# Performance work log

Measured on AMD Instinct MI355X. Metric: run time of the kernel, lower is better.

## Reference

```python
import jax, jax.numpy as jnp
import numpy as np

N_NODES = 100000
N_EDGES = 1600000
N_LABEL = 200000
HID = 128
OUT = 5


def setup_inputs() -> dict:
    key = jax.random.key(0)
    k1, k2, k3, k4, k5 = jax.random.split(key, 5)
    x = jax.random.normal(k1, (N_NODES, HID), dtype=jnp.float32)
    edge_index = jax.random.randint(k2, (2, N_EDGES), 0, N_NODES, dtype=jnp.int64)
    edge_label_index = jax.random.randint(k3, (2, N_LABEL), 0, N_NODES, dtype=jnp.int64)
    W_gcn = jax.random.normal(k4, (HID, HID), dtype=jnp.float32) / np.sqrt(HID)
    b_gcn = jnp.zeros((HID,), dtype=jnp.float32)
    W_lin = jax.random.normal(k5, (2 * HID, OUT), dtype=jnp.float32) / np.sqrt(2 * HID)
    b_lin = jnp.zeros((OUT,), dtype=jnp.float32)
    return {"x": x, "edge_index": edge_index, "edge_label_index": edge_label_index,
            "W_gcn": W_gcn, "b_gcn": b_gcn, "W_lin": W_lin, "b_lin": b_lin}


def _gcn_conv(x, edge_index, W, b):
    # PyG GCNConv defaults: add self-loops, symmetric normalization,
    # linear transform first, then scatter-add of norm * x[src] into dst.
    n = x.shape[0]
    loop = jnp.arange(n, dtype=edge_index.dtype)
    src = jnp.concatenate([edge_index[0], loop])  # [E+N]
    dst = jnp.concatenate([edge_index[1], loop])  # [E+N]
    xw = x @ W  # [N, H]
    ones = jnp.ones(src.shape[0], dtype=x.dtype)
    deg = jax.ops.segment_sum(ones, dst, num_segments=n)  # in-degree incl self-loop
    dinv = jnp.where(deg > 0, jax.lax.rsqrt(deg), 0.0)
    norm = dinv[src] * dinv[dst]  # [E+N]
    msgs = xw[src] * norm[:, None]  # [E+N, H] gather + scale
    out = jax.ops.segment_sum(msgs, dst, num_segments=n)  # scatter-add
    return out + b


def reference(x, edge_index, edge_label_index, W_gcn, b_gcn, W_lin, b_lin):
    h = _gcn_conv(x, edge_index, W_gcn, b_gcn)  # [N, H]
    drug_emb = h[edge_label_index[0]]  # [E_label, H]
    prot_emb = h[edge_label_index[1]]  # [E_label, H]
    edge_emb = jnp.concatenate([drug_emb, prot_emb], axis=1)  # [E_label, 2H]
    return edge_emb @ W_lin + b_lin  # [E_label, OUT]
```

## Files before the change

kernel.cpp:

```cpp
#include <hip/hip_runtime.h>

#define N_NODES 100000
#define N_EDGES 1600000
#define N_LABEL 200000
#define HID 128
#define OUT 5

#define NBUCK 391
#define EPB   2048
#define NBLK_E 782
#define PREC_BLKS 9


__device__ inline void bf2x(unsigned u, float& lo, float& hi) {
    lo = __uint_as_float(u << 16);
    hi = __uint_as_float(u & 0xffff0000u);
}
__device__ inline unsigned pack2(float a, float b) {
    unsigned ua = __float_as_uint(a), ub = __float_as_uint(b);
    ua = (ua + 0x7fffu + ((ua >> 16) & 1u)) >> 16;
    ub = (ub + 0x7fffu + ((ub >> 16) & 1u)) & 0xffff0000u;
    return ua | ub;
}

__global__ __launch_bounds__(256) void k_hist(const int* __restrict__ ei,
                                              int* __restrict__ hist,
                                              const float* __restrict__ Wg,
                                              const float* __restrict__ bg,
                                              const float* __restrict__ Wl,
                                              float* __restrict__ G) {
    const int t = threadIdx.x, b = blockIdx.x;
    if (b >= NBLK_E) {
        int o = (b - NBLK_E) * 256 + t;
        if (o < 129 * 16) {
            int r = o >> 4, jj = o & 15;
            float acc = 0.f;
            if (jj < 2 * OUT) {
                const int half = (jj >= OUT);
                const int j = half ? jj - OUT : jj;
                for (int c = 0; c < HID; ++c) {
                    float w2 = Wl[(half * HID + c) * OUT + j];
                    float a = (r < HID) ? Wg[r * HID + c] : bg[c];
                    acc += a * w2;
                }
            }
            G[o] = acc;
        }
        return;
    }
    __shared__ int h[NBUCK];
    for (int i = t; i < NBUCK; i += 256) h[i] = 0;
    __syncthreads();
    const int e0 = b * EPB;
#pragma unroll
    for (int i = 0; i < 8; ++i) {
        int e = e0 + i * 256 + t;
        if (e < N_EDGES) atomicAdd(&h[ei[N_EDGES + e] >> 8], 1);
    }
    __syncthreads();
    for (int i = t; i < NBUCK; i += 256) hist[i * NBLK_E + b] = h[i];
}

__global__ __launch_bounds__(256) void k_scanb(int* __restrict__ hist,
                                               int* __restrict__ btot,
                                               int* __restrict__ bbase,
                                               int* __restrict__ total) {
    __shared__ int part[256];
    const int b = blockIdx.x, t = threadIdx.x;
    int* row = hist + b * NBLK_E;
    const int lo = t * 4, hi = min(lo + 4, NBLK_E);
    int v[4]; int s = 0;
    for (int i = lo; i < hi; ++i) { v[i - lo] = row[i]; s += v[i - lo]; }
    part[t] = s;
    __syncthreads();
#pragma unroll
    for (int off = 1; off < 256; off <<= 1) {
        int a = (t >= off) ? part[t - off] : 0;
        __syncthreads();
        part[t] += a;
        __syncthreads();
    }
    int run = part[t] - s;
    for (int i = lo; i < hi; ++i) { int x = v[i - lo]; row[i] = run; run += x; }
    if (t == 255) {
        int tot = part[255];
        btot[b] = tot;
        bbase[b] = atomicAdd(total, tot);
    }
}

__global__ __launch_bounds__(256) void k_part(const int* __restrict__ ei,
                                              const int* __restrict__ hist,
                                              const int* __restrict__ bbase,
                                              unsigned* __restrict__ bedge) {
    __shared__ int cur[NBUCK];
    const int t = threadIdx.x, b = blockIdx.x;
    for (int i = t; i < NBUCK; i += 256) cur[i] = bbase[i] + hist[i * NBLK_E + b];
    __syncthreads();
    const int e0 = b * EPB;
#pragma unroll
    for (int i = 0; i < 8; ++i) {
        int e = e0 + i * 256 + t;
        if (e < N_EDGES) {
            int dst = ei[N_EDGES + e];
            unsigned src = (unsigned)ei[e];
            int pos = atomicAdd(&cur[dst >> 8], 1);
            bedge[pos] = src | ((unsigned)(dst & 255) << 20);
        }
    }
}

__global__ __launch_bounds__(256) void k_build(const unsigned* __restrict__ bedge,
                                               const int* __restrict__ bbase,
                                               const int* __restrict__ btot,
                                               int* __restrict__ csr,
                                               int2* __restrict__ seg,
                                               float* __restrict__ dinv) {
    __shared__ int cnt[256];
    __shared__ int nb[256];
    __shared__ int cursor[256];
    const int b = blockIdx.x, t = threadIdx.x;
    const int base = bbase[b];
    const int size = btot[b];
    cnt[t] = 0;
    __syncthreads();
    for (int i = t; i < size; i += 256) atomicAdd(&cnt[bedge[base + i] >> 20], 1);
    __syncthreads();
    const int c = cnt[t];
    nb[t] = c;
    __syncthreads();
#pragma unroll
    for (int off = 1; off < 256; off <<= 1) {
        int a = (t >= off) ? nb[t - off] : 0;
        __syncthreads();
        nb[t] += a;
        __syncthreads();
    }
    const int myBase = nb[t] - c;
    cursor[t] = myBase;
    __syncthreads();
    for (int i = t; i < size; i += 256) {
        unsigned v = bedge[base + i];
        int pos = atomicAdd(&cursor[v >> 20], 1);
        csr[base + pos] = (int)(v & 0xFFFFFu);
    }
    const int n = b * 256 + t;
    if (n < N_NODES) {
        seg[n] = make_int2(base + myBase, c);
        dinv[n] = rsqrtf((float)(c + 1));
    }
}

__global__ __launch_bounds__(256) void k_t(const float* __restrict__ x,
                                           const float* __restrict__ G,
                                           const float* __restrict__ dinv,
                                           unsigned* __restrict__ t16) {
    __shared__ float Gs[HID * 11];
    const int tid = threadIdx.x;
    for (int o = tid; o < HID * 10; o += 256) {
        int k = o / 10, j = o - k * 10;
        Gs[k * 11 + j] = G[k * 16 + j];
    }
    __syncthreads();

    int gid = blockIdx.x * 256 + tid;
    int n = gid >> 4;
    int i = gid & 15;

    float xv[8];
#pragma unroll
    for (int m = 0; m < 8; ++m) xv[m] = x[(size_t)n * HID + i + 16 * m];

    float p[10];
#pragma unroll
    for (int j = 0; j < 10; ++j) p[j] = 0.f;
#pragma unroll
    for (int m = 0; m < 8; ++m) {
        const float* g = &Gs[(i + 16 * m) * 11];
#pragma unroll
        for (int j = 0; j < 10; ++j) p[j] += xv[m] * g[j];
    }
#pragma unroll
    for (int off = 1; off < 16; off <<= 1) {
#pragma unroll
        for (int j = 0; j < 10; ++j) p[j] += __shfl_xor(p[j], off);
    }
    float va = (i == 0) ? p[0] : (i == 1) ? p[2] : (i == 2) ? p[4] : (i == 3) ? p[6] : p[8];
    float vb = (i == 0) ? p[1] : (i == 1) ? p[3] : (i == 2) ? p[5] : (i == 3) ? p[7] : p[9];
    float di = dinv[n];
    if (i < 5)      t16[(size_t)n * 8 + i] = pack2(di * va, di * vb);
    else if (i < 8) t16[(size_t)n * 8 + i] = 0u;
}

__global__ __launch_bounds__(256) void k_pullt(const unsigned* __restrict__ t16,
                                               const int2* __restrict__ seg,
                                               const int* __restrict__ csr,
                                               const float* __restrict__ dinv,
                                               const float* __restrict__ G,
                                               float* __restrict__ proj) {
    const int gid = blockIdx.x * 256 + threadIdx.x;
    const int n = gid >> 6;
    const int lane = gid & 63;
    const int e2 = lane >> 3;
    const int i = lane & 7;

    float aLo = 0.f, aHi = 0.f;
    if (e2 == 0) {
        bf2x(t16[(size_t)n * 8 + i], aLo, aHi);
    }

    const int2 sg = seg[n];
    const int beg = sg.x, deg = sg.y;

    for (int base = 0; base < deg; base += 64) {
        const int cnt = min(64, deg - base);
        int myIdx = (lane < cnt) ? csr[beg + base + lane] : 0;
        for (int j = 0; j * 8 < cnt; ++j) {
            int e = j * 8 + e2;
            int s = __shfl(myIdx, e);
            unsigned u = 0u;
            if (e < cnt) u = t16[(size_t)s * 8 + i];
            float lo, hi;
            bf2x(u, lo, hi);
            aLo += lo; aHi += hi;
        }
    }

    aLo += __shfl_xor(aLo, 8);  aHi += __shfl_xor(aHi, 8);
    aLo += __shfl_xor(aLo, 16); aHi += __shfl_xor(aHi, 16);
    aLo += __shfl_xor(aLo, 32); aHi += __shfl_xor(aHi, 32);

    if (lane < 5) {
        float di = dinv[n];
        float2 c0 = ((const float2*)(G + HID * 16))[lane];
        float2 r;
        r.x = di * aLo + c0.x;
        r.y = di * aHi + c0.y;
        *(float2*)&proj[(size_t)n * 16 + 2 * lane] = r;
    }
}

__global__ __launch_bounds__(256) void k_link2(const int* __restrict__ eli,
                                               const float* __restrict__ proj,
                                               const float* __restrict__ bl,
                                               float* __restrict__ out) {
    int t = blockIdx.x * 256 + threadIdx.x;
    int l = t >> 3, o = t & 7;
    if (l >= N_LABEL || o >= OUT) return;
    int d = eli[l];
    int p = eli[N_LABEL + l];
    out[l * OUT + o] = proj[d * 16 + o] + proj[p * 16 + OUT + o] + bl[o];
}

extern "C" void kernel_launch(void* const* d_in, const int* in_sizes, int n_in,
                              void* d_out, int out_size, void* d_ws, size_t ws_size,
                              hipStream_t stream) {
    const float* x     = (const float*)d_in[0];
    const int*   ei    = (const int*)d_in[1];
    const int*   eli   = (const int*)d_in[2];
    const float* W_gcn = (const float*)d_in[3];
    const float* b_gcn = (const float*)d_in[4];
    const float* W_lin = (const float*)d_in[5];
    const float* b_lin = (const float*)d_in[6];
    float* out = (float*)d_out;

    unsigned* t16    = (unsigned*)d_ws;
    float* proj      = (float*)(t16 + (size_t)N_NODES * 8);
    float* G         = proj + (size_t)N_NODES * 16;
    float* dinv      = G + 129 * 16;
    unsigned* bedge  = (unsigned*)(dinv + N_NODES);
    int*   csr       = (int*)(bedge + N_EDGES);
    int2*  seg       = (int2*)(csr + N_EDGES);
    int*   hist      = (int*)(seg + N_NODES);
    int*   btot      = hist + NBUCK * NBLK_E;
    int*   bbase     = btot + NBUCK;
    int*   total     = bbase + NBUCK;

    hipMemsetAsync(total, 0, sizeof(int), stream);

    k_hist<<<NBLK_E + PREC_BLKS, 256, 0, stream>>>(ei, hist, W_gcn, b_gcn, W_lin, G);
    k_scanb<<<NBUCK, 256, 0, stream>>>(hist, btot, bbase, total);
    k_part<<<NBLK_E, 256, 0, stream>>>(ei, hist, bbase, bedge);
    k_build<<<NBUCK, 256, 0, stream>>>(bedge, bbase, btot, csr, seg, dinv);
    k_t<<<N_NODES * 16 / 256, 256, 0, stream>>>(x, G, dinv, t16);
    k_pullt<<<N_NODES * 64 / 256, 256, 0, stream>>>(t16, seg, csr, dinv, G, proj);
    k_link2<<<(N_LABEL * 8 + 255) / 256, 256, 0, stream>>>(eli, proj, b_lin, out);
}
```

Before: 128.9 us.

## Replace CSR build and pull gather with bucketed shared-memory atomic accumulation

Drops the per-node CSR construction. Degrees are now counted from the dst-bucketed edge list, and aggregation becomes a per-bucket kernel that adds fp32 source rows into a 128-node shared-memory accumulator with LDS atomics. The bucket size shrinks from 256 to 128 nodes, which doubles the bucket count, and the bf16 packing of the projected features is replaced by full fp32 rows of 16 floats. This removes one scatter pass and the CSR/seg arrays, in exchange for doubled gather bytes per edge, shared-memory atomic contention, and only 782 aggregation blocks.

```diff
diff --git a/kernel.cpp b/kernel.cpp
--- a/kernel.cpp
+++ b/kernel.cpp
@@ -6,22 +6,13 @@
 #define HID 128
 #define OUT 5
 
-#define NBUCK 391
+#define BSH   7
+#define BSZ   128
+#define NBUCK 782
 #define EPB   2048
 #define NBLK_E 782
 #define PREC_BLKS 9
 
-
-__device__ inline void bf2x(unsigned u, float& lo, float& hi) {
-    lo = __uint_as_float(u << 16);
-    hi = __uint_as_float(u & 0xffff0000u);
-}
-__device__ inline unsigned pack2(float a, float b) {
-    unsigned ua = __float_as_uint(a), ub = __float_as_uint(b);
-    ua = (ua + 0x7fffu + ((ua >> 16) & 1u)) >> 16;
-    ub = (ub + 0x7fffu + ((ub >> 16) & 1u)) & 0xffff0000u;
-    return ua | ub;
-}
 
 __global__ __launch_bounds__(256) void k_hist(const int* __restrict__ ei,
                                               int* __restrict__ hist,
@@ -55,7 +46,7 @@
 #pragma unroll
     for (int i = 0; i < 8; ++i) {
         int e = e0 + i * 256 + t;
-        if (e < N_EDGES) atomicAdd(&h[ei[N_EDGES + e] >> 8], 1);
+        if (e < N_EDGES) atomicAdd(&h[ei[N_EDGES + e] >> BSH], 1);
     }
     __syncthreads();
     for (int i = t; i < NBUCK; i += 256) hist[i * NBLK_E + b] = h[i];
@@ -104,57 +95,33 @@
         if (e < N_EDGES) {
             int dst = ei[N_EDGES + e];
             unsigned src = (unsigned)ei[e];
-            int pos = atomicAdd(&cur[dst >> 8], 1);
-            bedge[pos] = src | ((unsigned)(dst & 255) << 20);
+            int pos = atomicAdd(&cur[dst >> BSH], 1);
+            bedge[pos] = src | ((unsigned)(dst & (BSZ - 1)) << 20);
         }
     }
 }
 
-__global__ __launch_bounds__(256) void k_build(const unsigned* __restrict__ bedge,
-                                               const int* __restrict__ bbase,
-                                               const int* __restrict__ btot,
-                                               int* __restrict__ csr,
-                                               int2* __restrict__ seg,
-                                               float* __restrict__ dinv) {
-    __shared__ int cnt[256];
-    __shared__ int nb[256];
-    __shared__ int cursor[256];
+__global__ __launch_bounds__(256) void k_deg(const unsigned* __restrict__ bedge,
+                                             const int* __restrict__ bbase,
+                                             const int* __restrict__ btot,
+                                             float* __restrict__ dinv) {
+    __shared__ int cnt[BSZ];
     const int b = blockIdx.x, t = threadIdx.x;
-    const int base = bbase[b];
-    const int size = btot[b];
-    cnt[t] = 0;
-    __syncthreads();
-    for (int i = t; i < size; i += 256) atomicAdd(&cnt[bedge[base + i] >> 20], 1);
-    __syncthreads();
-    const int c = cnt[t];
-    nb[t] = c;
-    __syncthreads();
-#pragma unroll
-    for (int off = 1; off < 256; off <<= 1) {
-        int a = (t >= off) ? nb[t - off] : 0;
-        __syncthreads();
-        nb[t] += a;
-        __syncthreads();
-    }
-    const int myBase = nb[t] - c;
-    cursor[t] = myBase;
-    __syncthreads();
-    for (int i = t; i < size; i += 256) {
-        unsigned v = bedge[base + i];
-        int pos = atomicAdd(&cursor[v >> 20], 1);
-        csr[base + pos] = (int)(v & 0xFFFFFu);
-    }
-    const int n = b * 256 + t;
-    if (n < N_NODES) {
-        seg[n] = make_int2(base + myBase, c);
-        dinv[n] = rsqrtf((float)(c + 1));
+    const int base = bbase[b], size = btot[b];
+    if (t < BSZ) cnt[t] = 0;
+    __syncthreads();
+    for (int e = t; e < size; e += 256) atomicAdd(&cnt[bedge[base + e] >> 20], 1);
+    __syncthreads();
+    if (t < BSZ) {
+        int n = b * BSZ + t;
+        if (n < N_NODES) dinv[n] = rsqrtf((float)(cnt[t] + 1));
     }
 }
 
 __global__ __launch_bounds__(256) void k_t(const float* __restrict__ x,
                                            const float* __restrict__ G,
                                            const float* __restrict__ dinv,
-                                           unsigned* __restrict__ t16) {
+                                           float* __restrict__ t) {
     __shared__ float Gs[HID * 11];
     const int tid = threadIdx.x;
     for (int o = tid; o < HID * 10; o += 256) {
@@ -185,58 +152,57 @@
 #pragma unroll
         for (int j = 0; j < 10; ++j) p[j] += __shfl_xor(p[j], off);
     }
-    float va = (i == 0) ? p[0] : (i == 1) ? p[2] : (i == 2) ? p[4] : (i == 3) ? p[6] : p[8];
-    float vb = (i == 0) ? p[1] : (i == 1) ? p[3] : (i == 2) ? p[5] : (i == 3) ? p[7] : p[9];
-    float di = dinv[n];
-    if (i < 5)      t16[(size_t)n * 8 + i] = pack2(di * va, di * vb);
-    else if (i < 8) t16[(size_t)n * 8 + i] = 0u;
-}
-
-__global__ __launch_bounds__(256) void k_pullt(const unsigned* __restrict__ t16,
-                                               const int2* __restrict__ seg,
-                                               const int* __restrict__ csr,
+    float val = (i == 0) ? p[0] : (i == 1) ? p[1] : (i == 2) ? p[2] : (i == 3) ? p[3] :
+                (i == 4) ? p[4] : (i == 5) ? p[5] : (i == 6) ? p[6] : (i == 7) ? p[7] :
+                (i == 8) ? p[8] : (i == 9) ? p[9] : 0.f;
+    t[(size_t)n * 16 + i] = dinv[n] * val;
+}
+
+__global__ __launch_bounds__(256) void k_accum(const unsigned* __restrict__ bedge,
+                                               const int* __restrict__ bbase,
+                                               const int* __restrict__ btot,
+                                               const float* __restrict__ t,
                                                const float* __restrict__ dinv,
                                                const float* __restrict__ G,
                                                float* __restrict__ proj) {
-    const int gid = blockIdx.x * 256 + threadIdx.x;
-    const int n = gid >> 6;
-    const int lane = gid & 63;
-    const int e2 = lane >> 3;
-    const int i = lane & 7;
-
-    float aLo = 0.f, aHi = 0.f;
-    if (e2 == 0) {
-        bf2x(t16[(size_t)n * 8 + i], aLo, aHi);
-    }
-
-    const int2 sg = seg[n];
-    const int beg = sg.x, deg = sg.y;
-
-    for (int base = 0; base < deg; base += 64) {
-        const int cnt = min(64, deg - base);
-        int myIdx = (lane < cnt) ? csr[beg + base + lane] : 0;
-        for (int j = 0; j * 8 < cnt; ++j) {
-            int e = j * 8 + e2;
-            int s = __shfl(myIdx, e);
-            unsigned u = 0u;
-            if (e < cnt) u = t16[(size_t)s * 8 + i];
-            float lo, hi;
-            bf2x(u, lo, hi);
-            aLo += lo; aHi += hi;
-        }
-    }
-
-    aLo += __shfl_xor(aLo, 8);  aHi += __shfl_xor(aHi, 8);
-    aLo += __shfl_xor(aLo, 16); aHi += __shfl_xor(aHi, 16);
-    aLo += __shfl_xor(aLo, 32); aHi += __shfl_xor(aHi, 32);
-
-    if (lane < 5) {
-        float di = dinv[n];
-        float2 c0 = ((const float2*)(G + HID * 16))[lane];
-        float2 r;
-        r.x = di * aLo + c0.x;
-        r.y = di * aHi + c0.y;
-        *(float2*)&proj[(size_t)n * 16 + 2 * lane] = r;
+    __shared__ float acc[BSZ][17];
+    const int b = blockIdx.x, tid = threadIdx.x;
+    const int base = bbase[b], size = btot[b];
+    const int g = tid >> 4;
+    const int i = tid & 15;
+
+    for (int r = g; r < BSZ; r += 16) {
+        int n = b * BSZ + r;
+        acc[r][i] = (n < N_NODES) ? t[(size_t)n * 16 + i] : 0.f;
+    }
+    __syncthreads();
+
+    int e = 0;
+    for (; e + 64 <= size; e += 64) {
+        unsigned w0 = bedge[base + e + g];
+        unsigned w1 = bedge[base + e + 16 + g];
+        unsigned w2 = bedge[base + e + 32 + g];
+        unsigned w3 = bedge[base + e + 48 + g];
+        float v0 = t[(size_t)(w0 & 0xFFFFFu) * 16 + i];
+        float v1 = t[(size_t)(w1 & 0xFFFFFu) * 16 + i];
+        float v2 = t[(size_t)(w2 & 0xFFFFFu) * 16 + i];
+        float v3 = t[(size_t)(w3 & 0xFFFFFu) * 16 + i];
+        atomicAdd(&acc[w0 >> 20][i], v0);
+        atomicAdd(&acc[w1 >> 20][i], v1);
+        atomicAdd(&acc[w2 >> 20][i], v2);
+        atomicAdd(&acc[w3 >> 20][i], v3);
+    }
+    for (int e2 = e + g; e2 < size; e2 += 16) {
+        unsigned w = bedge[base + e2];
+        float v = t[(size_t)(w & 0xFFFFFu) * 16 + i];
+        atomicAdd(&acc[w >> 20][i], v);
+    }
+    __syncthreads();
+
+    const float c0 = G[HID * 16 + i];
+    for (int r = g; r < BSZ; r += 16) {
+        int n = b * BSZ + r;
+        if (n < N_NODES) proj[(size_t)n * 16 + i] = dinv[n] * acc[r][i] + c0;
     }
 }
 
@@ -264,14 +230,12 @@
     const float* b_lin = (const float*)d_in[6];
     float* out = (float*)d_out;
 
-    unsigned* t16    = (unsigned*)d_ws;
-    float* proj      = (float*)(t16 + (size_t)N_NODES * 8);
+    float* t         = (float*)d_ws;
+    float* proj      = t + (size_t)N_NODES * 16;
     float* G         = proj + (size_t)N_NODES * 16;
     float* dinv      = G + 129 * 16;
     unsigned* bedge  = (unsigned*)(dinv + N_NODES);
-    int*   csr       = (int*)(bedge + N_EDGES);
-    int2*  seg       = (int2*)(csr + N_EDGES);
-    int*   hist      = (int*)(seg + N_NODES);
+    int*   hist      = (int*)(bedge + N_EDGES);
     int*   btot      = hist + NBUCK * NBLK_E;
     int*   bbase     = btot + NBUCK;
     int*   total     = bbase + NBUCK;
@@ -281,8 +245,8 @@
     k_hist<<<NBLK_E + PREC_BLKS, 256, 0, stream>>>(ei, hist, W_gcn, b_gcn, W_lin, G);
     k_scanb<<<NBUCK, 256, 0, stream>>>(hist, btot, bbase, total);
     k_part<<<NBLK_E, 256, 0, stream>>>(ei, hist, bbase, bedge);
-    k_build<<<NBUCK, 256, 0, stream>>>(bedge, bbase, btot, csr, seg, dinv);
-    k_t<<<N_NODES * 16 / 256, 256, 0, stream>>>(x, G, dinv, t16);
-    k_pullt<<<N_NODES * 64 / 256, 256, 0, stream>>>(t16, seg, csr, dinv, G, proj);
+    k_deg<<<NBUCK, 256, 0, stream>>>(bedge, bbase, btot, dinv);
+    k_t<<<N_NODES * 16 / 256, 256, 0, stream>>>(x, G, dinv, t);
+    k_accum<<<NBUCK, 256, 0, stream>>>(bedge, bbase, btot, t, dinv, G, proj);
     k_link2<<<(N_LABEL * 8 + 255) / 256, 256, 0, stream>>>(eli, proj, b_lin, out);
 }
```

New measurement: 269.8 us. +109.3%, slower.
